# Kernel optimization log

Hardware: AMD Instinct MI355X
Metric: run time of the kernel (lower is better)

## Reference

```python
import jax, jax.numpy as jnp
import numpy as np

NUM_HEADS = 16


def rotate_half(x):
    half = x.shape[-1] // 2
    return jnp.concatenate((-x[..., half:], x[..., :half]), axis=-1)


def rope_tables(seq_len, head_dim, dtype=jnp.float32):
    inv_freq = 1.0 / (10000.0 ** (jnp.arange(0, head_dim, 2, dtype=jnp.float32) / head_dim))
    t = jnp.arange(seq_len, dtype=jnp.float32)
    freqs = jnp.outer(t, inv_freq)                 # [S, hd/2]
    emb = jnp.concatenate((freqs, freqs), axis=-1)  # [S, hd]
    return jnp.cos(emb).astype(dtype), jnp.sin(emb).astype(dtype)


def setup_inputs() -> dict:
    key = jax.random.key(0)
    k1, k2, k3 = jax.random.split(key, 3)
    B, S, D = 2, 2048, 1024
    x = jax.random.normal(k1, (B, S, D), dtype=jnp.float32)
    # causal lower-triangular mask, broadcast over batch/heads
    mask = jnp.tril(jnp.ones((S, S), dtype=bool))[None, None, :, :]
    w_qkv = jax.random.normal(k2, (3 * D, D), dtype=jnp.float32) * (D ** -0.5)
    w_out = jax.random.normal(k3, (D, D), dtype=jnp.float32) * (D ** -0.5)
    return {"x": x, "mask": mask, "w_qkv": w_qkv, "w_out": w_out}


def reference(x, mask, w_qkv, w_out):
    B, S, D = x.shape
    H = NUM_HEADS
    hd = D // H
    scale = hd ** -0.5

    qkv = jnp.einsum('bsd,ed->bse', x, w_qkv)          # [B, S, 3D]
    q, k, v = jnp.split(qkv, 3, axis=-1)

    def split(t):
        return t.reshape(B, S, H, hd).transpose(0, 2, 1, 3)  # [B, H, S, hd]

    q, k, v = split(q), split(k), split(v)

    cos, sin = rope_tables(S, hd, x.dtype)             # [S, hd]
    cos = cos[None, None]
    sin = sin[None, None]
    q = q * cos + rotate_half(q) * sin
    k = k * cos + rotate_half(k) * sin

    attn = jnp.einsum('bhqd,bhkd->bhqk', q, k) * scale  # [B, H, S, S]
    attn = jnp.where(mask, attn, jnp.float32(-jnp.inf).astype(attn.dtype))
    attn = jax.nn.softmax(attn, axis=-1)
    out = jnp.einsum('bhqk,bhkd->bhqd', attn, v)        # [B, H, S, hd]
    out = out.transpose(0, 2, 1, 3).reshape(B, S, D)
    return jnp.einsum('bsd,ed->bse', out, w_out)
```

## Files before the change

kernel.cpp:

```cpp
#include <hip/hip_runtime.h>
#include <hip/hip_bf16.h>

typedef __attribute__((ext_vector_type(8))) __bf16 bf16x8;
typedef __attribute__((ext_vector_type(4))) __bf16 bf16x4;
typedef __attribute__((ext_vector_type(2))) __bf16 bf16x2;
typedef __attribute__((ext_vector_type(4))) float f32x4;
typedef __attribute__((ext_vector_type(16))) float f32x16;

#define SEQ 2048
#define NH 16
#define HD 64
#define DMODEL 1024
#define BATCH 2
#define MTOT 4096
#define NSLOT 72

#if __has_builtin(__builtin_amdgcn_exp2f)
#define EXP2(x) __builtin_amdgcn_exp2f(x)
#else
#define EXP2(x) exp2f(x)
#endif
#define MFMA32(a, b, c) __builtin_amdgcn_mfma_f32_32x32x16_bf16(a, b, c, 0, 0, 0)

__device__ __forceinline__ void gl_lds16(const void* g, void* l) {
    __builtin_amdgcn_global_load_lds(
        (const __attribute__((address_space(1))) void*)(uintptr_t)g,
        (__attribute__((address_space(3))) void*)(uintptr_t)l,
        16, 0, 0);
}

__device__ __forceinline__ unsigned pk2(float x, float y) {
    union { bf16x2 h; unsigned u; } c;
    c.h = bf16x2{ (__bf16)x, (__bf16)y };
    return c.u;
}

#define TILE_SYNC(N) do {                                           \
    asm volatile("s_waitcnt vmcnt(" #N ")" ::: "memory");           \
    __builtin_amdgcn_s_barrier();                                   \
    __builtin_amdgcn_sched_barrier(0);                              \
} while (0)

__constant__ int4 FITEM[80] = {
    {31,0,16,68},{31,16,32,69},{31,32,48,70},{31,48,64,71},
    {23,0,16,37},{23,16,32,38},{23,32,48,39},
    {15,0,16,14},{15,16,32,15},
    {30,15,31,65},{30,46,62,67},
    {22,30,46,36},
    {7,0,16,-1},
    {29,0,15,60},{29,15,30,61},{29,30,45,62},{29,45,60,63},
    {30,0,15,64},{30,31,46,66},
    {22,0,15,34},{22,15,30,35},
    {21,14,29,32},{21,29,44,33},
    {28,14,29,57},{28,43,58,59},
    {14,0,15,12},{14,15,30,13},
    {27,0,14,52},{27,14,28,53},{27,28,42,54},{27,42,56,55},
    {28,0,14,56},{28,29,43,58},
    {20,0,14,28},{20,14,28,29},{20,28,42,30},
    {21,0,14,31},
    {26,13,27,49},{26,40,54,51},
    {19,26,40,27},
    {13,0,14,10},{13,14,28,11},
    {6,0,14,-1},
    {25,0,13,44},{25,13,26,45},{25,26,39,46},{25,39,52,47},
    {26,0,13,48},{26,27,40,50},
    {24,12,25,41},{24,37,50,43},
    {19,0,13,25},{19,13,26,26},
    {18,12,25,23},{18,25,38,24},
    {12,0,13,8},{12,13,26,9},
    {24,0,12,40},{24,25,37,42},
    {17,0,12,19},{17,12,24,20},{17,24,36,21},
    {18,0,12,22},
    {16,22,34,18},
    {11,0,12,6},{11,12,24,7},
    {5,0,12,-1},
    {16,0,11,16},{16,11,22,17},
    {10,0,11,4},{10,11,22,5},
    {9,0,10,2},{9,10,20,3},
    {4,0,10,-1},
    {8,0,9,0},{8,9,18,1},
    {3,0,8,-1},{2,0,6,-1},{1,0,4,-1},{0,0,2,-1}
};

__global__ __launch_bounds__(256) void cast3(const float4* __restrict__ x,
                                             const float4* __restrict__ wq,
                                             const float4* __restrict__ wo,
                                             __bf16* __restrict__ xb,
                                             __bf16* __restrict__ wqb,
                                             __bf16* __restrict__ wob) {
    const int NX  = 1024 * 1024;
    const int NWQ = 768 * 1024;
    const int NTOT = NX + NWQ + 256 * 1024;
    int i = blockIdx.x * 256 + threadIdx.x;
    if (i >= NTOT) return;
    float4 v; __bf16* dst; int j;
    if (i < NX)            { j = i;            v = x[j];  dst = xb;  }
    else if (i < NX + NWQ) { j = i - NX;       v = wq[j]; dst = wqb; }
    else                   { j = i - NX - NWQ; v = wo[j]; dst = wob; }
    bf16x4 o = { (__bf16)v.x, (__bf16)v.y, (__bf16)v.z, (__bf16)v.w };
    *(bf16x4*)(dst + (size_t)j * 4) = o;
}

__global__ __launch_bounds__(512, 2) void gemm_qkv(const __bf16* __restrict__ A,
                                                   const __bf16* __restrict__ Bt,
                                                   __bf16* __restrict__ Qp,
                                                   char* __restrict__ K2,
                                                   char* __restrict__ V2) {
    const int K = 1024;
    __shared__ __align__(16) char lds[3 * 49152];
    const int tid = threadIdx.x, lane = tid & 63, wave = tid >> 6;
    const int lrow = lane & 15, quad = lane >> 4;
    const int bx = blockIdx.x, by = blockIdx.y;
    const int m0 = by * 256, n0 = bx * 128;
    const int wm = wave >> 1, wn = wave & 1;

    const __bf16* ap[4]; int aof[4];
    const __bf16* bp[2]; int bof[2];
#pragma unroll
    for (int i = 0; i < 4; ++i) {
        int r0 = i * 64 + wave * 8;
        int row = r0 + (lane >> 3);
        int cg = (lane & 7) ^ (row & 7);
        ap[i] = A + (size_t)(m0 + row) * K + cg * 8;
        aof[i] = r0 * 128;
    }
#pragma unroll
    for (int i = 0; i < 2; ++i) {
        int r0 = i * 64 + wave * 8;
        int row = r0 + (lane >> 3);
        int cg = (lane & 7) ^ (row & 7);
        bp[i] = Bt + (size_t)(n0 + row) * K + cg * 8;
        bof[i] = 32768 + r0 * 128;
    }
    int arow[4], brow[4];
#pragma unroll
    for (int i = 0; i < 4; ++i) {
        arow[i] = wm * 64 + i * 16 + lrow;
        brow[i] = wn * 64 + i * 16 + lrow;
    }

    f32x4 z = {0.f, 0.f, 0.f, 0.f};
    f32x4 acc[4][4];
#pragma unroll
    for (int i = 0; i < 4; ++i)
#pragma unroll
        for (int j = 0; j < 4; ++j) acc[i][j] = z;

    auto STAGE = [&](char* base, int k0) {
#pragma unroll
        for (int i = 0; i < 4; ++i) gl_lds16(ap[i] + k0, base + aof[i]);
#pragma unroll
        for (int i = 0; i < 2; ++i) gl_lds16(bp[i] + k0, base + bof[i]);
    };
    auto COMPUTE = [&](const char* base) {
        const char* bb = base + 32768;
#pragma unroll
        for (int ks = 0; ks < 2; ++ks) {
            bf16x8 af[4], bfr[4];
#pragma unroll
            for (int i = 0; i < 4; ++i)
                af[i] = *(const bf16x8*)(base + arow[i] * 128 +
                                         (((ks * 4 + quad) ^ (arow[i] & 7)) << 4));
#pragma unroll
            for (int i = 0; i < 4; ++i)
                bfr[i] = *(const bf16x8*)(bb + brow[i] * 128 +
                                          (((ks * 4 + quad) ^ (brow[i] & 7)) << 4));
            __builtin_amdgcn_s_setprio(1);
#pragma unroll
            for (int i = 0; i < 4; ++i)
#pragma unroll
                for (int j = 0; j < 4; ++j)
                    acc[i][j] = __builtin_amdgcn_mfma_f32_16x16x32_bf16(
                        af[i], bfr[j], acc[i][j], 0, 0, 0);
            __builtin_amdgcn_s_setprio(0);
        }
    };

    STAGE(lds, 0);
    STAGE(lds + 49152, 64);
    TILE_SYNC(6);
    for (int t = 0; t < 14; ++t) {
        STAGE(lds + ((t + 2) % 3) * 49152, (t + 2) * 64);
        COMPUTE(lds + (t % 3) * 49152);
        TILE_SYNC(6);
    }
    COMPUTE(lds + 2 * 49152);
    TILE_SYNC(0);
    COMPUTE(lds);

    const int nt = bx;
    const int sec = nt >> 3;
    const int b = m0 >> 11;
    const int s0b = m0 & (SEQ - 1);
    const int h = (nt & 7) * 2 + wn;
    const int bh = b * NH + h;

    if (sec < 2) {
        const float scale = sec ? 1.0f : 0.18033688011112042f;
        char* Kb = K2 + (size_t)bh * 262144;
        float invf0 = 0.15915494309189535f *
                      exp2f(-(float)lrow * 0.4152410118609203f);
        float invf1 = invf0 * 0.01f;
#pragma unroll
        for (int i = 0; i < 4; ++i) {
            int srow0 = s0b + wm * 64 + i * 16 + quad * 4;
#pragma unroll
            for (int j = 0; j < 2; ++j) {
                float invf = j ? invf1 : invf0;
                int hdlo = j * 16 + lrow;
#pragma unroll
                for (int r = 0; r < 4; ++r) {
                    int s = srow0 + r;
                    float rev = (float)s * invf;
                    float fr = rev - floorf(rev);
                    float sn = __builtin_amdgcn_sinf(fr);
                    float cs = __builtin_amdgcn_cosf(fr);
                    float lo = acc[i][j][r], hi = acc[i][j + 2][r];
                    float olo = (lo * cs - hi * sn) * scale;
                    float ohi = (hi * cs + lo * sn) * scale;
                    if (sec == 0) {
                        size_t base = ((size_t)bh * SEQ + s) * HD + hdlo;
                        Qp[base] = (__bf16)olo;
                        Qp[base + 32] = (__bf16)ohi;
                    } else {
                        char* kt = Kb + (s >> 5) * 4096 + (s & 31) * 16 +
                                   ((lrow >> 3) & 1) * 512 + (lrow & 7) * 2;
                        *(__bf16*)(kt + j * 1024) = (__bf16)olo;
                        *(__bf16*)(kt + (j + 2) * 1024) = (__bf16)ohi;
                    }
                }
            }
        }
    } else {
        char* Vb = V2 + (size_t)bh * 262144;
#pragma unroll
        for (int i = 0; i < 4; ++i) {
            int srow0 = s0b + wm * 64 + i * 16 + quad * 4;
            int kb = srow0 >> 4, ko = srow0 & 15;
            int slot0 = ((ko >> 2) & 1) * 8 + (ko >> 3) * 4;
#pragma unroll
            for (int j = 0; j < 4; ++j) {
                int ch = j * 16 + lrow;
                bf16x4 wv = { (__bf16)acc[i][j][0], (__bf16)acc[i][j][1],
                              (__bf16)acc[i][j][2], (__bf16)acc[i][j][3] };
                *(bf16x4*)(Vb + kb * 2048 + ch * 32 + slot0 * 2) = wv;
            }
        }
    }
}

__global__ __launch_bounds__(256) void gemm_bt(const __bf16* __restrict__ A,
                                               const __bf16* __restrict__ Bt,
                                               float* __restrict__ Cf,
                                               int M, int N, int K) {
    __shared__ __bf16 sA[2][128 * 64];
    __shared__ __bf16 sB[2][128 * 64];
    const int tid = threadIdx.x, lane = tid & 63, wave = tid >> 6;
    const int lrow = lane & 15, quad = lane >> 4;

    int lin = blockIdx.y * 8 + blockIdx.x;
    lin = (lin & 7) * 32 + (lin >> 3);
    const int bx = lin & 7, by = lin >> 3;
    const int m0 = by * 128, n0 = bx * 128;
    const int wm = wave >> 1, wn = wave & 1;

    const __bf16* ap[4]; const __bf16* bp[4]; int ldso[4];
#pragma unroll
    for (int i = 0; i < 4; ++i) {
        int r0 = i * 32 + wave * 8;
        int row = r0 + (lane >> 3);
        int cg = (lane & 7) ^ (row & 7);
        ap[i] = A + (size_t)(m0 + row) * K + cg * 8;
        bp[i] = Bt + (size_t)(n0 + row) * K + cg * 8;
        ldso[i] = r0 * 128;
    }
    int arow[4], brow[4];
#pragma unroll
    for (int i = 0; i < 4; ++i) {
        arow[i] = wm * 64 + i * 16 + lrow;
        brow[i] = wn * 64 + i * 16 + lrow;
    }

    f32x4 z = {0.f, 0.f, 0.f, 0.f};
    f32x4 acc[4][4];
#pragma unroll
    for (int i = 0; i < 4; ++i)
#pragma unroll
        for (int j = 0; j < 4; ++j) acc[i][j] = z;

    char* sA0 = (char*)sA[0]; char* sA1 = (char*)sA[1];
    char* sB0 = (char*)sB[0]; char* sB1 = (char*)sB[1];

    auto STAGE = [&](char* dA, char* dB, int k0) {
#pragma unroll
        for (int i = 0; i < 4; ++i) gl_lds16(ap[i] + k0, dA + ldso[i]);
#pragma unroll
        for (int i = 0; i < 4; ++i) gl_lds16(bp[i] + k0, dB + ldso[i]);
    };
    auto COMPUTE = [&](const char* sAb, const char* sBb) {
#pragma unroll
        for (int ks = 0; ks < 2; ++ks) {
            bf16x8 af[4], bfr[4];
#pragma unroll
            for (int i = 0; i < 4; ++i)
                af[i] = *(const bf16x8*)(sAb + arow[i] * 128 +
                                         (((ks * 4 + quad) ^ (arow[i] & 7)) << 4));
#pragma unroll
            for (int i = 0; i < 4; ++i)
                bfr[i] = *(const bf16x8*)(sBb + brow[i] * 128 +
                                          (((ks * 4 + quad) ^ (brow[i] & 7)) << 4));
#pragma unroll
            for (int i = 0; i < 4; ++i)
#pragma unroll
                for (int j = 0; j < 4; ++j)
                    acc[i][j] = __builtin_amdgcn_mfma_f32_16x16x32_bf16(
                        af[i], bfr[j], acc[i][j], 0, 0, 0);
        }
    };

    STAGE(sA0, sB0, 0);
    __syncthreads();
    for (int k0 = 0; k0 < K; k0 += 128) {
        if (k0 + 64 < K) STAGE(sA1, sB1, k0 + 64);
        COMPUTE(sA0, sB0);
        __syncthreads();
        if (k0 + 128 < K) STAGE(sA0, sB0, k0 + 128);
        COMPUTE(sA1, sB1);
        __syncthreads();
    }
#pragma unroll
    for (int i = 0; i < 4; ++i)
#pragma unroll
        for (int j = 0; j < 4; ++j)
#pragma unroll
            for (int r = 0; r < 4; ++r) {
                int row = m0 + wm * 64 + i * 16 + quad * 4 + r;
                int col = n0 + wn * 64 + j * 16 + lrow;
                Cf[(size_t)row * N + col] = acc[i][j][r];
            }
}

__global__ __launch_bounds__(64) void flash_attn(const __bf16* __restrict__ Qp,
                                                 const char* __restrict__ K2,
                                                 const char* __restrict__ V2,
                                                 __bf16* __restrict__ Aout,
                                                 __bf16* __restrict__ Opart,
                                                 float* __restrict__ Lpart) {
    const int lane = threadIdx.x;
    const int ql = lane & 31, half = lane >> 5;
    const int bh = blockIdx.x;
    const int4 it = FITEM[blockIdx.y];
    const int s = it.x, t0 = it.y, t1 = it.z, slot = it.w;
    const int b = bh >> 4, hh = bh & 15;

    const __bf16* qb = Qp + ((size_t)bh * SEQ + s * 64 + ql) * HD + half * 8;
    bf16x8 qf0[4], qf1[4];
#pragma unroll
    for (int kc = 0; kc < 4; ++kc) {
        qf0[kc] = *(const bf16x8*)(qb + kc * 16);
        qf1[kc] = *(const bf16x8*)(qb + 32 * HD + kc * 16);
    }
    const char* Kb = K2 + (size_t)bh * 262144 + half * 512 + ql * 16;
    const char* Vb = V2 + (size_t)bh * 262144 + ql * 32 + half * 16;

    f32x16 zz = {0.f};
    f32x16 oA0 = zz, oA1 = zz, oB0 = zz, oB1 = zz;
    float lA = 0.f, lB = 0.f;
    const int dA = 2 * s, dB = 2 * s + 1;
    const int thr = ql - 4 * half;

    auto STEP = [&](int t, const bf16x8* kf, bf16x8* kn) {
        bf16x8 vf[2][2];
#pragma unroll
        for (int lo = 0; lo < 2; ++lo) {
            const char* vp = Vb + (t * 2 + lo) * 2048;
            vf[lo][0] = *(const bf16x8*)(vp);
            vf[lo][1] = *(const bf16x8*)(vp + 1024);
        }
        if (t + 1 < t1) {
            const char* kt = Kb + (t + 1) * 4096;
#pragma unroll
            for (int kc = 0; kc < 4; ++kc)
                kn[kc] = *(const bf16x8*)(kt + kc * 1024);
        }
        const bool do0 = (t != dB);
        f32x16 st0 = zz, st1 = zz;
        if (do0) {
#pragma unroll
            for (int kc = 0; kc < 4; ++kc)
                st0 = MFMA32(kf[kc], qf0[kc], st0);
        }
#pragma unroll
        for (int kc = 0; kc < 4; ++kc)
            st1 = MFMA32(kf[kc], qf1[kc], st1);

        if (do0) {
#pragma unroll
            for (int i = 0; i < 16; ++i) st0[i] = EXP2(st0[i]);
            if (t == dA) {
#pragma unroll
                for (int g = 0; g < 4; ++g)
#pragma unroll
                    for (int tt = 0; tt < 4; ++tt)
                        if (8 * g + tt > thr) st0[g * 4 + tt] = 0.f;
            }
#pragma unroll
            for (int i = 0; i < 16; ++i) lA += st0[i];
        }
#pragma unroll
        for (int i = 0; i < 16; ++i) st1[i] = EXP2(st1[i]);
        if (t == dB) {
#pragma unroll
            for (int g = 0; g < 4; ++g)
#pragma unroll
                for (int tt = 0; tt < 4; ++tt)
                    if (8 * g + tt > thr) st1[g * 4 + tt] = 0.f;
        }
#pragma unroll
        for (int i = 0; i < 16; ++i) lB += st1[i];

#pragma unroll
        for (int lo = 0; lo < 2; ++lo) {
            if (do0) {
                union { unsigned u[4]; bf16x8 v; } p0;
#pragma unroll
                for (int d = 0; d < 4; ++d)
                    p0.u[d] = pk2(st0[lo * 8 + 2 * d], st0[lo * 8 + 2 * d + 1]);
                oA0 = MFMA32(vf[lo][0], p0.v, oA0);
                oA1 = MFMA32(vf[lo][1], p0.v, oA1);
            }
            union { unsigned u[4]; bf16x8 v; } p1;
#pragma unroll
            for (int d = 0; d < 4; ++d)
                p1.u[d] = pk2(st1[lo * 8 + 2 * d], st1[lo * 8 + 2 * d + 1]);
            oB0 = MFMA32(vf[lo][0], p1.v, oB0);
            oB1 = MFMA32(vf[lo][1], p1.v, oB1);
        }
    };

    bf16x8 kA[4], kB[4];
    {
        const char* kt = Kb + t0 * 4096;
#pragma unroll
        for (int kc = 0; kc < 4; ++kc)
            kA[kc] = *(const bf16x8*)(kt + kc * 1024);
    }
    int t = t0;
    while (true) {
        STEP(t, kA, kB);
        if (++t >= t1) break;
        STEP(t, kB, kA);
        if (++t >= t1) break;
    }

    lA += __shfl_xor(lA, 32, 64);
    lB += __shfl_xor(lB, 32, 64);

    if (slot < 0) {
        float iA = 1.0f / lA, iB = 1.0f / lB;
        __bf16* oa = Aout + ((size_t)b * SEQ + s * 64 + ql) * DMODEL + hh * HD;
        __bf16* ob = oa + (size_t)32 * DMODEL;
#pragma unroll
        for (int g = 0; g < 4; ++g) {
            bf16x4 wA0 = { (__bf16)(oA0[g*4+0]*iA), (__bf16)(oA0[g*4+1]*iA),
                           (__bf16)(oA0[g*4+2]*iA), (__bf16)(oA0[g*4+3]*iA) };
            bf16x4 wA1 = { (__bf16)(oA1[g*4+0]*iA), (__bf16)(oA1[g*4+1]*iA),
                           (__bf16)(oA1[g*4+2]*iA), (__bf16)(oA1[g*4+3]*iA) };
            bf16x4 wB0 = { (__bf16)(oB0[g*4+0]*iB), (__bf16)(oB0[g*4+1]*iB),
                           (__bf16)(oB0[g*4+2]*iB), (__bf16)(oB0[g*4+3]*iB) };
            bf16x4 wB1 = { (__bf16)(oB1[g*4+0]*iB), (__bf16)(oB1[g*4+1]*iB),
                           (__bf16)(oB1[g*4+2]*iB), (__bf16)(oB1[g*4+3]*iB) };
            *(bf16x4*)(oa + 8 * g + 4 * half) = wA0;
            *(bf16x4*)(oa + 32 + 8 * g + 4 * half) = wA1;
            *(bf16x4*)(ob + 8 * g + 4 * half) = wB0;
            *(bf16x4*)(ob + 32 + 8 * g + 4 * half) = wB1;
        }
    } else {
        __bf16* oa = Opart + ((size_t)(bh * NSLOT + slot) << 12) + ql * 64;
        __bf16* ob = oa + 32 * 64;
#pragma unroll
        for (int g = 0; g < 4; ++g) {
            bf16x4 wA0 = { (__bf16)oA0[g*4+0], (__bf16)oA0[g*4+1],
                           (__bf16)oA0[g*4+2], (__bf16)oA0[g*4+3] };
            bf16x4 wA1 = { (__bf16)oA1[g*4+0], (__bf16)oA1[g*4+1],
                           (__bf16)oA1[g*4+2], (__bf16)oA1[g*4+3] };
            bf16x4 wB0 = { (__bf16)oB0[g*4+0], (__bf16)oB0[g*4+1],
                           (__bf16)oB0[g*4+2], (__bf16)oB0[g*4+3] };
            bf16x4 wB1 = { (__bf16)oB1[g*4+0], (__bf16)oB1[g*4+1],
                           (__bf16)oB1[g*4+2], (__bf16)oB1[g*4+3] };
            *(bf16x4*)(oa + 8 * g + 4 * half) = wA0;
            *(bf16x4*)(oa + 32 + 8 * g + 4 * half) = wA1;
            *(bf16x4*)(ob + 8 * g + 4 * half) = wB0;
            *(bf16x4*)(ob + 32 + 8 * g + 4 * half) = wB1;
        }
        if (!half) {
            Lpart[(bh * NSLOT + slot) * 64 + ql] = lA;
            Lpart[(bh * NSLOT + slot) * 64 + 32 + ql] = lB;
        }
    }
}

__global__ __launch_bounds__(256) void combine(const __bf16* __restrict__ Opart,
                                               const float* __restrict__ Lpart,
                                               __bf16* __restrict__ Aout) {
    const int bh = blockIdx.x;
    const int s = 8 + blockIdx.y;
    const int C = (s < 16) ? 2 : ((s < 24) ? 3 : 4);
    const int base = (s < 16) ? (s - 8) * 2
                   : (s < 24) ? 16 + (s - 16) * 3
                              : 40 + (s - 24) * 4;
    const int t = threadIdx.x;
    const int r = t >> 2, cg = (t & 3) * 16;
    float acc[16];
#pragma unroll
    for (int i = 0; i < 16; ++i) acc[i] = 0.f;
    float l = 0.f;
    for (int ci = 0; ci < C; ++ci) {
        int ch = bh * NSLOT + base + ci;
        l += Lpart[ch * 64 + r];
        const __bf16* p = Opart + ((size_t)ch << 12) + r * 64 + cg;
#pragma unroll
        for (int k = 0; k < 2; ++k) {
            bf16x8 v = ((const bf16x8*)p)[k];
#pragma unroll
            for (int j = 0; j < 8; ++j) acc[k * 8 + j] += (float)v[j];
        }
    }
    float invl = 1.0f / l;
    const int b = bh >> 4, hh = bh & 15;
    __bf16* dst = Aout + ((size_t)(b * SEQ + s * 64 + r)) * DMODEL +
                  hh * 64 + cg;
#pragma unroll
    for (int k = 0; k < 2; ++k) {
        bf16x8 w;
#pragma unroll
        for (int j = 0; j < 8; ++j) w[j] = (__bf16)(acc[k * 8 + j] * invl);
        ((bf16x8*)dst)[k] = w;
    }
}

extern "C" void kernel_launch(void* const* d_in, const int* in_sizes, int n_in,
                              void* d_out, int out_size, void* d_ws, size_t ws_size,
                              hipStream_t stream) {
    (void)in_sizes; (void)n_in; (void)out_size; (void)ws_size;
    const float* x  = (const float*)d_in[0];
    const float* wq = (const float*)d_in[2];
    const float* wo = (const float*)d_in[3];
    float* out = (float*)d_out;

    char* w = (char*)d_ws;
    __bf16* xb   = (__bf16*)(w);
    __bf16* wqb  = (__bf16*)(w + (8ull << 20));
    __bf16* wob  = (__bf16*)(w + (14ull << 20));
    __bf16* Opart= (__bf16*)(w + (16ull << 20));
    float*  Lpart= (float*) (w + (35ull << 20));
    __bf16* Qb   = (__bf16*)(w + (40ull << 20));
    char*   K2   = (char*)  (w + (48ull << 20));
    char*   V2   = (char*)  (w + (56ull << 20));
    __bf16* aob  = xb;

    cast3<<<8192, 256, 0, stream>>>((const float4*)x, (const float4*)wq,
                                    (const float4*)wo, xb, wqb, wob);
    gemm_qkv<<<dim3(24, 16), 512, 0, stream>>>(xb, wqb, Qb, K2, V2);
    flash_attn<<<dim3(32, 80), 64, 0, stream>>>(Qb, K2, V2, aob, Opart, Lpart);
    combine<<<dim3(32, 24), 256, 0, stream>>>(Opart, Lpart, aob);
    gemm_bt<<<dim3(8, 32), 256, 0, stream>>>(aob, wob, out, MTOT, 1024, 1024);
}
```

Before: 184.7 us.

## Split flash-attention KV loop across four waves with LDS reduction

Each flash attention block now runs four waves instead of one. The waves interleave over the key tiles with a stride of four, and waves 1-3 then stash their partial O accumulators and row sums in LDS for wave 0 to add up before the normal output path. This shortens the serial KV loop per block and adds parallelism. The cost is 48KB of LDS per block, a barrier, and a reduction step. It relies on a fixed softmax max (no rescaling), so plain summation of the partials is valid.

After: 208.8 us. 1.13x slower.

```diff
diff --git a/kernel.cpp b/kernel.cpp
--- a/kernel.cpp
+++ b/kernel.cpp
@@ -340,13 +340,15 @@
             }
 }
 
-__global__ __launch_bounds__(64) void flash_attn(const __bf16* __restrict__ Qp,
-                                                 const char* __restrict__ K2,
-                                                 const char* __restrict__ V2,
-                                                 __bf16* __restrict__ Aout,
-                                                 __bf16* __restrict__ Opart,
-                                                 float* __restrict__ Lpart) {
-    const int lane = threadIdx.x;
+__global__ __launch_bounds__(256) void flash_attn(const __bf16* __restrict__ Qp,
+                                                  const char* __restrict__ K2,
+                                                  const char* __restrict__ V2,
+                                                  __bf16* __restrict__ Aout,
+                                                  __bf16* __restrict__ Opart,
+                                                  float* __restrict__ Lpart) {
+    __shared__ __align__(16) char lds[49152 + 768];
+    const int tid = threadIdx.x;
+    const int lane = tid & 63, wave = tid >> 6;
     const int ql = lane & 31, half = lane >> 5;
     const int bh = blockIdx.x;
     const int4 it = FITEM[blockIdx.y];
@@ -377,8 +379,8 @@
             vf[lo][0] = *(const bf16x8*)(vp);
             vf[lo][1] = *(const bf16x8*)(vp + 1024);
         }
-        if (t + 1 < t1) {
-            const char* kt = Kb + (t + 1) * 4096;
+        if (t + 4 < t1) {
+            const char* kt = Kb + (t + 4) * 4096;
 #pragma unroll
             for (int kc = 0; kc < 4; ++kc)
                 kn[kc] = *(const bf16x8*)(kt + kc * 1024);
@@ -438,23 +440,59 @@
         }
     };
 
-    bf16x8 kA[4], kB[4];
-    {
-        const char* kt = Kb + t0 * 4096;
-#pragma unroll
-        for (int kc = 0; kc < 4; ++kc)
-            kA[kc] = *(const bf16x8*)(kt + kc * 1024);
-    }
-    int t = t0;
-    while (true) {
-        STEP(t, kA, kB);
-        if (++t >= t1) break;
-        STEP(t, kB, kA);
-        if (++t >= t1) break;
+    int t = t0 + wave;
+    if (t < t1) {
+        bf16x8 kA[4], kB[4];
+        {
+            const char* kt = Kb + t * 4096;
+#pragma unroll
+            for (int kc = 0; kc < 4; ++kc)
+                kA[kc] = *(const bf16x8*)(kt + kc * 1024);
+        }
+        while (true) {
+            STEP(t, kA, kB);
+            t += 4; if (t >= t1) break;
+            STEP(t, kB, kA);
+            t += 4; if (t >= t1) break;
+        }
     }
 
     lA += __shfl_xor(lA, 32, 64);
     lB += __shfl_xor(lB, 32, 64);
+
+    if (wave) {
+        char* base = lds + (wave - 1) * 16384 + lane * 16;
+#define STASH(A, a) {                                                       \
+    _Pragma("unroll")                                                       \
+    for (int c = 0; c < 4; ++c) {                                           \
+        f32x4 v = { A[c*4+0], A[c*4+1], A[c*4+2], A[c*4+3] };               \
+        *(f32x4*)(base + (a) * 4096 + c * 1024) = v;                        \
+    } }
+        STASH(oA0, 0) STASH(oA1, 1) STASH(oB0, 2) STASH(oB1, 3)
+#undef STASH
+        if (!half) {
+            *(float*)(lds + 49152 + (wave - 1) * 256 + ql * 4) = lA;
+            *(float*)(lds + 49152 + (wave - 1) * 256 + 128 + ql * 4) = lB;
+        }
+    }
+    __syncthreads();
+    if (wave != 0) return;
+
+#pragma unroll
+    for (int w = 0; w < 3; ++w) {
+        const char* pb = lds + w * 16384 + lane * 16;
+#define GATHER(A, a) {                                                      \
+    _Pragma("unroll")                                                       \
+    for (int c = 0; c < 4; ++c) {                                           \
+        f32x4 r = *(const f32x4*)(pb + (a) * 4096 + c * 1024);              \
+        A[c*4+0] += r[0]; A[c*4+1] += r[1];                                 \
+        A[c*4+2] += r[2]; A[c*4+3] += r[3];                                 \
+    } }
+        GATHER(oA0, 0) GATHER(oA1, 1) GATHER(oB0, 2) GATHER(oB1, 3)
+#undef GATHER
+        lA += *(const float*)(lds + 49152 + w * 256 + ql * 4);
+        lB += *(const float*)(lds + 49152 + w * 256 + 128 + ql * 4);
+    }
 
     if (slot < 0) {
         float iA = 1.0f / lA, iB = 1.0f / lB;
@@ -562,7 +600,7 @@
     cast3<<<8192, 256, 0, stream>>>((const float4*)x, (const float4*)wq,
                                     (const float4*)wo, xb, wqb, wob);
     gemm_qkv<<<dim3(24, 16), 512, 0, stream>>>(xb, wqb, Qb, K2, V2);
-    flash_attn<<<dim3(32, 80), 64, 0, stream>>>(Qb, K2, V2, aob, Opart, Lpart);
+    flash_attn<<<dim3(32, 80), 256, 0, stream>>>(Qb, K2, V2, aob, Opart, Lpart);
     combine<<<dim3(32, 24), 256, 0, stream>>>(Opart, Lpart, aob);
     gemm_bt<<<dim3(8, 32), 256, 0, stream>>>(aob, wob, out, MTOT, 1024, 1024);
 }
```
